# Performance work log

Hardware: AMD Instinct MI355X
Metric: run time of the kernel (lower is better)

Reference implementation:

```python
import jax, jax.numpy as jnp
import numpy as np

B, N, H, D, F = 32, 128, 256, 256, 512   # batch, nodes, gru hidden, latent dim, mlp hidden
SUP = 0.5                                 # ancestor_suppression_strength
EPS = 1e-6


def _gru(x, h, Wx, Wh, bx, bh):
    """torch.nn.GRUCell math; x,h: [..., H]."""
    gx = x @ Wx + bx
    gh = h @ Wh + bh
    rx, ux, nx = jnp.split(gx, 3, axis=-1)
    rh, uh, nh = jnp.split(gh, 3, axis=-1)
    r = jax.nn.sigmoid(rx + rh)
    u = jax.nn.sigmoid(ux + uh)
    n = jnp.tanh(nx + r * nh)
    return (1.0 - u) * n + u * h


def setup_inputs() -> dict:
    key = jax.random.key(0)
    ks = jax.random.split(key, 12)
    rn = lambda k, shape, fan: jax.random.normal(k, shape, jnp.float32) * (fan ** -0.5)
    return {
        "z": jax.random.normal(ks[0], (B, D), jnp.float32),
        "targets": jax.random.randint(ks[1], (B, N, N), 0, 2, jnp.int32),
        "W_init": rn(ks[2], (D, H), D),
        "b_init": jnp.zeros((H,), jnp.float32),
        "Wx": rn(ks[3], (H, 3 * H), H),
        "Wh": rn(ks[4], (H, 3 * H), H),
        "bx": jnp.zeros((3 * H,), jnp.float32),
        "bh": jnp.zeros((3 * H,), jnp.float32),
        "W1": rn(ks[5], (2 * H + D, F), 2 * H + D),
        "b1": jnp.zeros((F,), jnp.float32),
        "W2": rn(ks[6], (F, 1), F),
        "b2": jnp.zeros((1,), jnp.float32),
    }


def reference(z, targets, W_init, b_init, Wx, Wh, bx, bh, W1, b1, W2, b2):
    # teacher-forcing link targets: strictly lower-triangular (parents have smaller index)
    tgt = jnp.tril(targets.astype(jnp.float32), k=-1)  # [B,N,N]
    idx = jnp.arange(N)

    def decode_one(z1, t1):  # z1:[D], t1:[N,N]
        h0 = jnp.tanh(z1 @ W_init + b_init)                      # decoder_init: z -> node-0 state
        states0 = jnp.zeros((N, H), jnp.float32).at[0].set(h0)
        A0 = jnp.zeros((N, N), jnp.float32)                      # ancestor bitset: A[i,j]=1 iff j ancestor of i

        def step(carry, t):
            states, A, ll = carry
            m = (idx < t).astype(jnp.float32)                    # existing-node mask
            pooled = (states * m[:, None]).sum(0) / m.sum()      # mean aggregation
            h_prov = _gru(pooled, h0, Wx, Wh, bx, bh)            # provisional new-node state
            # parent logits: MLP([h_new, h_j, z]) for every existing node j
            feat = jnp.concatenate([jnp.broadcast_to(h_prov, (N, H)), states,
                                    jnp.broadcast_to(z1, (N, D))], axis=-1)   # [N, 2H+D]
            logits = (jax.nn.relu(feat @ W1 + b1) @ W2 + b2)[:, 0]            # [N]
            row = t1[t]                                          # teacher-forced parents of node t
            anc = jnp.minimum(row @ A, 1.0)                      # j already ancestor of a chosen parent
            q = jnp.clip(jax.nn.sigmoid(logits) * (1.0 - SUP * anc), EPS, 1.0 - EPS)
            ll = ll + (m * (row * jnp.log(q) + (1.0 - row) * jnp.log1p(-q))).sum()
            A = A.at[t].set(jnp.minimum(row + row @ A, 1.0))     # ancestors(t) = parents U their ancestors
            states = states.at[t].set(h_prov)
            m2 = (idx <= t).astype(jnp.float32)[:, None]
            pooled2 = (states * m2).sum(0) / m2.sum()
            upd = _gru(jnp.broadcast_to(pooled2, (N, H)), states, Wx, Wh, bx, bh)
            states = m2 * upd + (1.0 - m2) * states              # propagate info among generated nodes
            return (states, A, ll), None

        (states, A, ll), _ = jax.lax.scan(step, (states0, A0, jnp.zeros((), jnp.float32)),
                                          jnp.arange(1, N))
        return t1, ll                                            # link matrix (teacher forced), log-likelihood

    L, ll = jax.vmap(decode_one)(z, tgt)
    return L, ll
```

## Files before the change

kernel.cpp:

```cpp
#include <hip/hip_runtime.h>
#include <hip/hip_bf16.h>
#include <math.h>

#define Bz 32
#define Nn 128
#define Hh 256
#define Dd 256
#define Ff 512
#define Gg 768
#define NT 512

typedef short v8s __attribute__((ext_vector_type(8)));
typedef float f4  __attribute__((ext_vector_type(4)));
#define MFMA(a,b,c) __builtin_amdgcn_mfma_f32_16x16x32_bf16(a,b,c,0,0,0)

#define WS_H0    0
#define WS_GH0   (WS_H0 + Bz*Hh)
#define WS_ZW1   (WS_GH0 + Bz*Gg)
#define WS_GXP   (WS_ZW1 + Bz*Ff)
#define WS_LOGP  (WS_GXP + Bz*2*8*Gg)
#define WS_BAR   (WS_LOGP + Bz*2*8*Nn)
#define WS_XS    (WS_BAR + Bz*32)
#define WS_WB    (WS_XS + Bz*16384)

#define SM_SW    0
#define SM_SST   81920
#define SM_NLDS  147456
#define SM_GXF   155648
#define SM_HPF   158720
#define SM_GX2   159232
#define SM_GHT   159616
#define SM_BASE  160000
#define SM_BHS   160256
#define SM_PSN   160640
#define SM_LOGI  160768
#define SM_RBIT  161280
#define SM_ANCW  161312
#define SM_AMASK 161376
#define SMEM_SZ  163424

__device__ __forceinline__ unsigned short f2bf(float x) {
  unsigned u = __float_as_uint(x);
  u = u + 0x7fffu + ((u >> 16) & 1u);
  return (unsigned short)(u >> 16);
}
__device__ __forceinline__ unsigned pack2(float e, float o) {
  return (unsigned)f2bf(e) | ((unsigned)f2bf(o) << 16);
}
__device__ __forceinline__ unsigned pkbf(float x, float y) {
  __hip_bfloat162 h = __float22bfloat162_rn(make_float2(x, y));
  union { __hip_bfloat162 h; unsigned u; } c; c.h = h; return c.u;
}
__device__ __forceinline__ float bf2f(unsigned short s) {
  return __uint_as_float(((unsigned)s) << 16);
}
__device__ __forceinline__ float sigm(float x) { return 1.0f / (1.0f + __expf(-x)); }
__device__ __forceinline__ float tanh_fast(float x) { return 2.0f / (1.0f + __expf(-2.0f*x)) - 1.0f; }
__device__ __forceinline__ v8s u4v(uint4 q) { union { uint4 q; v8s v; } c; c.q = q; return c.v; }

__device__ __forceinline__ void ast32(unsigned* p, unsigned v) {
  __hip_atomic_store(p, v, __ATOMIC_RELAXED, __HIP_MEMORY_SCOPE_AGENT);
}
__device__ __forceinline__ unsigned ald32(const unsigned* p) {
  return __hip_atomic_load(p, __ATOMIC_RELAXED, __HIP_MEMORY_SCOPE_AGENT);
}
__device__ __forceinline__ void ast64(unsigned long long* p, unsigned long long v) {
  __hip_atomic_store(p, v, __ATOMIC_RELAXED, __HIP_MEMORY_SCOPE_AGENT);
}
__device__ __forceinline__ unsigned long long ald64(const unsigned long long* p) {
  return __hip_atomic_load(p, __ATOMIC_RELAXED, __HIP_MEMORY_SCOPE_AGENT);
}

__device__ __forceinline__ void bbar(unsigned* cnt, unsigned& seq)
{
  __builtin_amdgcn_s_waitcnt(0x0F70);
  __syncthreads();
  seq += 8;
  if (threadIdx.x == 0) {
    __hip_atomic_fetch_add(cnt, 1u, __ATOMIC_RELAXED, __HIP_MEMORY_SCOPE_AGENT);
    while (__hip_atomic_load(cnt, __ATOMIC_RELAXED, __HIP_MEMORY_SCOPE_AGENT) < seq)
      __builtin_amdgcn_s_sleep(1);
  }
  __syncthreads();
}

__global__ void __launch_bounds__(256) prep_init(
    const int* __restrict__ tg, const float* __restrict__ Wx,
    const float* __restrict__ Wh, const float* __restrict__ W1,
    float* __restrict__ ws, float* __restrict__ out)
{
  const int stride = gridDim.x * blockDim.x;
  const int t0 = blockIdx.x * blockDim.x + threadIdx.x;

  for (int i = t0; i < Bz*Nn*Nn; i += stride) {
    int col = i & (Nn-1), row = (i >> 7) & (Nn-1);
    out[i] = (col < row) ? (float)tg[i] : 0.0f;
  }
  for (int i = t0; i < Bz; i += stride) out[Bz*Nn*Nn + i] = 0.0f;

  unsigned* BARu = (unsigned*)(ws + WS_BAR);
  for (int i = t0; i < Bz*32; i += stride) BARu[i] = 0u;

  unsigned* Wb = (unsigned*)(ws + WS_WB);
  for (int i = t0; i < 160*2048; i += stride) {
    int jw = i & 3, l = (i >> 2) & 63, ks = (i >> 8) & 7, nt = i >> 11;
    int k = ks*32 + (l >> 4)*8 + 2*jw;
    int n16 = l & 15;
    float lo, hi;
    if (nt < 48)       { int c = nt*16 + n16;        lo = Wh[k*Gg + c];      hi = Wh[(k+1)*Gg + c]; }
    else if (nt < 80)  { int f = (nt-48)*16 + n16;   lo = W1[(Hh+k)*Ff + f]; hi = W1[(Hh+k+1)*Ff + f]; }
    else if (nt < 128) { int c = (nt-80)*16 + n16;   lo = Wx[k*Gg + c];      hi = Wx[(k+1)*Gg + c]; }
    else               { int f = (nt-128)*16 + n16;  lo = W1[k*Ff + f];      hi = W1[(k+1)*Ff + f]; }
    Wb[i] = pack2(lo, hi);
  }
}

__global__ void __launch_bounds__(256) prep_batch(
    const float* __restrict__ z, const float* __restrict__ Wi,
    const float* __restrict__ bi, const float* __restrict__ Wh,
    const float* __restrict__ bh, const float* __restrict__ W1,
    float* __restrict__ ws)
{
  const int b = blockIdx.x, tid = threadIdx.x;
  __shared__ float zs[Dd], h0s[Hh];
  zs[tid] = z[b*Dd + tid];
  __syncthreads();
  float acc = bi[tid];
  for (int d = 0; d < Dd; ++d) acc = fmaf(zs[d], Wi[d*Hh + tid], acc);
  const float h0 = tanhf(acc);
  h0s[tid] = h0;
  ws[WS_H0 + b*Hh + tid] = h0;
  __syncthreads();
  for (int g = tid; g < Gg; g += 256) {
    float a = bh[g];
    for (int h = 0; h < Hh; ++h) a = fmaf(h0s[h], Wh[h*Gg + g], a);
    ws[WS_GH0 + b*Gg + g] = a;
  }
  for (int f = tid; f < Ff; f += 256) {
    float a = 0.0f;
    for (int d = 0; d < Dd; ++d) a = fmaf(zs[d], W1[(2*Hh + d)*Ff + f], a);
    ws[WS_ZW1 + b*Ff + f] = a;
  }
}

__device__ __forceinline__ void G_mfma(const unsigned short* SST, const uint4* SW4,
    int mt0, bool do1, int lane, f4* acc)
{
  #pragma unroll
  for (int ks = 0; ks < 8; ++ks) {
    const v8s a0 = *(const v8s*)(SST + (mt0*8 + ks)*512 + lane*8);
    const v8s w0 = u4v(SW4[(0*8 + ks)*64 + lane]);
    const v8s w1 = u4v(SW4[(1*8 + ks)*64 + lane]);
    const v8s w2 = u4v(SW4[(2*8 + ks)*64 + lane]);
    const v8s w3 = u4v(SW4[(3*8 + ks)*64 + lane]);
    const v8s w4 = u4v(SW4[(4*8 + ks)*64 + lane]);
    const v8s w5 = u4v(SW4[(5*8 + ks)*64 + lane]);
    acc[0] = MFMA(a0,w0,acc[0]); acc[1] = MFMA(a0,w1,acc[1]);
    acc[2] = MFMA(a0,w2,acc[2]); acc[3] = MFMA(a0,w3,acc[3]);
    acc[4] = MFMA(a0,w4,acc[4]); acc[5] = MFMA(a0,w5,acc[5]);
    if (do1) {
      const v8s a1 = *(const v8s*)(SST + ((mt0+1)*8 + ks)*512 + lane*8);
      acc[6]  = MFMA(a1,w0,acc[6]);  acc[7]  = MFMA(a1,w1,acc[7]);
      acc[8]  = MFMA(a1,w2,acc[8]);  acc[9]  = MFMA(a1,w3,acc[9]);
      acc[10] = MFMA(a1,w4,acc[10]); acc[11] = MFMA(a1,w5,acc[11]);
    }
  }
}

__device__ __forceinline__ void G_epi(const f4* ac, int mt, int t, int r,
    int quad, int c16, int lane, const float* GX2, const float* BHS,
    const unsigned short* SST, unsigned short* NLDS, float* PSN)
{
  #pragma unroll
  for (int ct = 0; ct < 2; ++ct) {
    const int hcl = ct*16 + c16;
    const f4 cr = ac[0 + ct], cu = ac[2 + ct], cn = ac[4 + ct];
    const float gxr = GX2[hcl], gxu = GX2[32+hcl], gxn = GX2[64+hcl];
    const float bhr = BHS[hcl], bhu = BHS[32+hcl], bhn = BHS[64+hcl];
    float colsum = 0.0f;
    #pragma unroll
    for (int rg = 0; rg < 4; ++rg) {
      const int row = mt*16 + quad*4 + rg;
      if (row < t) {
        const int spi = ((hcl>>3)*16 + quad*4 + rg)*8 + (hcl & 7);
        const float old = bf2f(SST[(mt*8 + r)*512 + spi]);
        const float rv = sigm(gxr + cr[rg] + bhr);
        const float uv = sigm(gxu + cu[rg] + bhu);
        const float nv = tanh_fast(gxn + rv*(cn[rg] + bhn));
        const float ns = (1.0f-uv)*nv + uv*old;
        NLDS[mt*512 + spi] = f2bf(ns);
        colsum += ns;
      }
    }
    colsum += __shfl_down(colsum, 16);
    colsum += __shfl_down(colsum, 32);
    if (lane < 16) atomicAdd(&PSN[ct*16 + lane], colsum);
  }
}

__device__ __forceinline__ void L_mfma(const unsigned short* SST, const uint4* SW4,
    int mt0, bool do1, int lane, f4* acc)
{
  #pragma unroll
  for (int ks = 0; ks < 8; ++ks) {
    const v8s a0 = *(const v8s*)(SST + (mt0*8 + ks)*512 + lane*8);
    const v8s c0 = u4v(SW4[(6*8 + ks)*64 + lane]);
    const v8s c1 = u4v(SW4[(7*8 + ks)*64 + lane]);
    const v8s c2 = u4v(SW4[(8*8 + ks)*64 + lane]);
    const v8s c3 = u4v(SW4[(9*8 + ks)*64 + lane]);
    acc[0] = MFMA(a0,c0,acc[0]); acc[1] = MFMA(a0,c1,acc[1]);
    acc[2] = MFMA(a0,c2,acc[2]); acc[3] = MFMA(a0,c3,acc[3]);
    if (do1) {
      const v8s a1 = *(const v8s*)(SST + ((mt0+1)*8 + ks)*512 + lane*8);
      acc[4] = MFMA(a1,c0,acc[4]); acc[5] = MFMA(a1,c1,acc[5]);
      acc[6] = MFMA(a1,c2,acc[6]); acc[7] = MFMA(a1,c3,acc[7]);
    }
  }
}

__device__ __forceinline__ void L_epi(const f4* ac, int mt, int t,
    int quad, int c16, const float* BASE, const float* w2r, float* LOGI)
{
  #pragma unroll
  for (int rg = 0; rg < 4; ++rg) {
    float v = fmaxf(ac[0][rg] + BASE[c16],    0.0f)*w2r[0]
            + fmaxf(ac[1][rg] + BASE[16+c16], 0.0f)*w2r[1]
            + fmaxf(ac[2][rg] + BASE[32+c16], 0.0f)*w2r[2]
            + fmaxf(ac[3][rg] + BASE[48+c16], 0.0f)*w2r[3];
    v += __shfl_xor(v, 1); v += __shfl_xor(v, 2);
    v += __shfl_xor(v, 4); v += __shfl_xor(v, 8);
    const int row = mt*16 + quad*4 + rg;
    if (c16 == 0 && row < t) atomicAdd(&LOGI[row], v);
  }
}

__global__ void __launch_bounds__(NT) decoder_main(
    const int* __restrict__ tg,
    const float* __restrict__ bx, const float* __restrict__ bh,
    const float* __restrict__ b1, const float* __restrict__ W2,
    const float* __restrict__ b2,
    float* __restrict__ ws, float* __restrict__ out)
{
  const int blk = blockIdx.x;
  const int b = blk & 31, r = blk >> 5;
  const int tid = threadIdx.x;
  const int lane = tid & 63, wv = tid >> 6;
  const int c16 = lane & 15, quad = lane >> 4;

  extern __shared__ char smem[];
  uint4* SW4 = (uint4*)(smem + SM_SW);
  unsigned short* SST = (unsigned short*)(smem + SM_SST);
  unsigned long long* SST64 = (unsigned long long*)(smem + SM_SST);
  unsigned short* NLDS = (unsigned short*)(smem + SM_NLDS);
  unsigned* NLDSu = (unsigned*)(smem + SM_NLDS);
  unsigned long long* NLDS64 = (unsigned long long*)(smem + SM_NLDS);
  float* GXF  = (float*)(smem + SM_GXF);
  unsigned short* HPF = (unsigned short*)(smem + SM_HPF);
  float* GX2  = (float*)(smem + SM_GX2);
  float* GHT  = (float*)(smem + SM_GHT);
  float* BASE = (float*)(smem + SM_BASE);
  float* BHS  = (float*)(smem + SM_BHS);
  float* PSN  = (float*)(smem + SM_PSN);
  float* LOGI = (float*)(smem + SM_LOGI);
  unsigned* RBIT  = (unsigned*)(smem + SM_RBIT);
  unsigned* ANCW  = (unsigned*)(smem + SM_ANCW);
  unsigned* AMASK = (unsigned*)(smem + SM_AMASK);

  const float* __restrict__ h0g  = ws + WS_H0  + b*Hh;
  const float* __restrict__ gh0g = ws + WS_GH0 + b*Gg;
  const float* __restrict__ zW1g = ws + WS_ZW1 + b*Ff;
  unsigned* GXPb = (unsigned*)(ws + WS_GXP) + b*2*8*Gg;
  unsigned* LOGPb = (unsigned*)(ws + WS_LOGP) + b*2*8*Nn;
  unsigned* bar = (unsigned*)(ws + WS_BAR) + b*32;
  unsigned long long* XS64 = (unsigned long long*)(ws + WS_XS) + b*8192;
  const uint4* WB4 = (const uint4*)(ws + WS_WB);

  for (int i = tid; i < 16384; i += NT) ((unsigned*)SST)[i] = 0u;
  for (int i = tid; i < 4096; i += NT) NLDSu[i] = 0u;
  for (int i = tid; i < 5120; i += NT) {
    const int lt = i >> 9, q = i & 511;
    int gt;
    if (lt < 6) { const int gate = lt >> 1, tt = lt & 1; gt = gate*16 + 2*r + tt; }
    else        { gt = 48 + 4*r + (lt - 6); }
    SW4[lt*512 + q] = WB4[gt*512 + q];
  }
  for (int i = tid; i < Nn*4; i += NT) AMASK[i] = 0u;
  if (tid < 96) BHS[tid] = bh[(tid >> 5)*256 + 32*r + (tid & 31)];
  float w2r[4];
  #pragma unroll
  for (int ft = 0; ft < 4; ++ft) w2r[ft] = W2[64*r + ft*16 + c16];
  const float b2v = b2[0];
  float p_bx[3][4], p_gh[3][4], p_h0[4];
  if (wv >= 6) {
    #pragma unroll
    for (int k = 0; k < 4; ++k) {
      const int c = 4*lane + k;
      p_h0[k] = h0g[c];
      #pragma unroll
      for (int g3 = 0; g3 < 3; ++g3) {
        p_bx[g3][k] = bx[g3*256 + c];
        p_gh[g3][k] = gh0g[g3*256 + c];
      }
    }
  }
  unsigned bseq = 0;
  __syncthreads();
  if (tid < Hh) {
    const int c = tid;
    SST[(c>>5)*512 + ((c>>3)&3)*128 + (c&7)] = f2bf(h0g[c]);
  }
  if (tid < 32) PSN[tid] = h0g[32*r + tid];
  __syncthreads();
  {
    union { unsigned u[4]; v8s v; } cv;
    const float4 a0 = *(const float4*)(PSN + quad*8);
    const float4 a1 = *(const float4*)(PSN + quad*8 + 4);
    cv.u[0] = pkbf(a0.x, a0.y); cv.u[1] = pkbf(a0.z, a0.w);
    cv.u[2] = pkbf(a1.x, a1.y); cv.u[3] = pkbf(a1.z, a1.w);
    const v8s avp = cv.v;
    unsigned* GXPw = GXPb + 1*8*Gg + r*Gg;
    #pragma unroll
    for (int k2 = 0; k2 < 6; ++k2) {
      const int nt = wv*6 + k2;
      f4 c = {0.0f,0.0f,0.0f,0.0f};
      c = MFMA(avp, u4v(WB4[(80 + nt)*512 + r*64 + lane]), c);
      if (quad == 0) ast32(GXPw + nt*16 + c16, __float_as_uint(c[0]));
    }
  }
  if (tid < 128) ast64(XS64 + r*128 + tid, SST64[r*128 + tid]);
  bbar(bar, bseq);

  for (int t = 1; t < Nn; ++t) {
    const int tpar = t & 1;
    const float invt  = 1.0f / (float)t;
    const float invt1 = 1.0f / (float)(t + 1);
    const int Mr   = (t + 15) >> 4;
    const int Mtot = (t + 16) >> 4;
    const int mtc  = t >> 4;
    const int nG = (Mr + 1) >> 1, nL = (Mr + 1) >> 1;
    const int njobs = nG + nL;

    for (int i = tid; i < Mr*1024; i += NT) {
      if (((i >> 7) & 7) != r) SST64[i] = ald64(XS64 + i);
    }
    if (tid < 384) {
      const unsigned long long* GXPr =
          (const unsigned long long*)(GXPb + tpar*8*Gg);
      float s0 = 0.0f, s1 = 0.0f;
      #pragma unroll
      for (int rr = 0; rr < 8; ++rr) {
        const unsigned long long v = ald64(GXPr + rr*384 + tid);
        s0 += __uint_as_float((unsigned)v);
        s1 += __uint_as_float((unsigned)(v >> 32));
      }
      GXF[2*tid]   = s0;
      GXF[2*tid+1] = s1;
    } else {
      const int j = tid - 384;
      const int val = (j < t) ? tg[b*Nn*Nn + t*Nn + j] : 0;
      const unsigned long long bal = __ballot(val != 0);
      if (lane == 0) {
        RBIT[tpar*4 + (wv-6)*2]     = (unsigned)bal;
        RBIT[tpar*4 + (wv-6)*2 + 1] = (unsigned)(bal >> 32);
      }
      LOGI[j] = 0.0f;
      if (j < 32) PSN[j] = 0.0f;
      unsigned m0=0,m1=0,m2=0,m3=0;
      if (j < t && val != 0) {
        m0 = AMASK[j*4+0]; m1 = AMASK[j*4+1];
        m2 = AMASK[j*4+2]; m3 = AMASK[j*4+3];
      }
      #pragma unroll
      for (int off = 1; off < 64; off <<= 1) {
        m0 |= __shfl_xor(m0, off); m1 |= __shfl_xor(m1, off);
        m2 |= __shfl_xor(m2, off); m3 |= __shfl_xor(m3, off);
      }
      if (lane == 0) {
        unsigned* aw = ANCW + tpar*8 + (wv-6)*4;
        aw[0] = m0; aw[1] = m1; aw[2] = m2; aw[3] = m3;
      }
    }
    __syncthreads();

    f4 acc[12];
    #pragma unroll
    for (int i = 0; i < 12; ++i) acc[i] = (f4){0.0f,0.0f,0.0f,0.0f};
    bool haveA = false, d1A = false; int kindA = 0, mtA = 0;
    if (wv < 6) {
      if (wv < njobs && wv < 6) {
        haveA = true;
        if (wv < nG) { kindA = 0; mtA = 2*wv;       d1A = (mtA + 1 < Mr); }
        else         { kindA = 1; mtA = 2*(wv-nG);  d1A = (mtA + 1 < Mr); }
        if (kindA == 0) G_mfma(SST, SW4, mtA, d1A, lane, acc);
        else            L_mfma(SST, SW4, mtA, d1A, lane, acc);
      }
    } else {
      if (wv == 6 && lane < 4)
        AMASK[t*4 + lane] = RBIT[tpar*4 + lane] | ANCW[tpar*8 + lane] | ANCW[tpar*8 + 4 + lane];
      if ((t & 15) == 0) {
        for (int q = tid - 384; q < 256; q += 128) NLDSu[mtc*256 + q] = 0u;
      }
      float hp[4];
      #pragma unroll
      for (int k = 0; k < 4; ++k) {
        const int c = 4*lane + k;
        const float rv = sigm(GXF[c]*invt       + p_bx[0][k] + p_gh[0][k]);
        const float uv = sigm(GXF[256+c]*invt   + p_bx[1][k] + p_gh[1][k]);
        const float nv = tanh_fast(GXF[512+c]*invt + p_bx[2][k] + rv*p_gh[2][k]);
        hp[k] = (1.0f - uv)*nv + uv*p_h0[k];
      }
      uint2 pk;
      pk.x = pack2(hp[0], hp[1]); pk.y = pack2(hp[2], hp[3]);
      *(uint2*)((unsigned short*)HPF + 4*lane) = pk;
      v8s av[8];
      #pragma unroll
      for (int ks = 0; ks < 8; ++ks) av[ks] = *(const v8s*)(HPF + ks*32 + quad*8);
      for (int j = wv - 6; j < 16; j += 2) {
        f4 c = {0.0f,0.0f,0.0f,0.0f};
        if (j < 6) {
          #pragma unroll
          for (int ks = 0; ks < 8; ++ks) c = MFMA(av[ks], u4v(SW4[(j*8 + ks)*64 + lane]), c);
          if (quad == 0) GHT[(j>>1)*32 + (j&1)*16 + c16] = c[0];
        } else if (j < 12) {
          const int jx = j - 6, g = jx >> 1, tt = jx & 1;
          const uint4* Bp = WB4 + (80 + g*16 + 2*r + tt)*512 + lane;
          #pragma unroll
          for (int ks = 0; ks < 8; ++ks) c = MFMA(av[ks], u4v(Bp[ks*64]), c);
          if (quad == 0) {
            const int col = g*256 + 32*r + tt*16 + c16;
            GX2[g*32 + tt*16 + c16] = (c[0] + GXF[col])*invt1 + bx[col];
          }
        } else {
          const int ft = j - 12;
          const uint4* Bp = WB4 + (128 + 4*r + ft)*512 + lane;
          #pragma unroll
          for (int ks = 0; ks < 8; ++ks) c = MFMA(av[ks], u4v(Bp[ks*64]), c);
          if (quad == 0) {
            const int f = 64*r + ft*16 + c16;
            BASE[ft*16 + c16] = c[0] + zW1g[f] + b1[f];
          }
        }
      }
    }
    __syncthreads();

    if (wv < 6) {
      if (haveA) {
        if (kindA == 0) {
          G_epi(acc,     mtA,   t, r, quad, c16, lane, GX2, BHS, SST, NLDS, PSN);
          if (d1A) G_epi(acc+6, mtA+1, t, r, quad, c16, lane, GX2, BHS, SST, NLDS, PSN);
        } else {
          L_epi(acc,     mtA,   t, quad, c16, BASE, w2r, LOGI);
          if (d1A) L_epi(acc+4, mtA+1, t, quad, c16, BASE, w2r, LOGI);
        }
      }
      if (wv < 2) {
        const int jB = 6 + wv;
        if (jB < njobs) {
          const int mtB = 2*(jB - nG);
          const bool d1B = (mtB + 1 < Mr);
          f4 acc2[8];
          #pragma unroll
          for (int i = 0; i < 8; ++i) acc2[i] = (f4){0.0f,0.0f,0.0f,0.0f};
          L_mfma(SST, SW4, mtB, d1B, lane, acc2);
          L_epi(acc2,     mtB,   t, quad, c16, BASE, w2r, LOGI);
          if (d1B) L_epi(acc2+4, mtB+1, t, quad, c16, BASE, w2r, LOGI);
        }
      }
    } else if (wv == 6 && lane < 32) {
      const int hcl = lane;
      const float rv = sigm(GX2[hcl]    + GHT[hcl]    + BHS[hcl]);
      const float uv = sigm(GX2[32+hcl] + GHT[32+hcl] + BHS[32+hcl]);
      const float nv = tanh_fast(GX2[64+hcl] + rv*(GHT[64+hcl] + BHS[64+hcl]));
      const float old = bf2f(HPF[32*r + hcl]);
      const float ns = (1.0f - uv)*nv + uv*old;
      const int spi = ((hcl>>3)*16 + (t & 15))*8 + (hcl & 7);
      NLDS[mtc*512 + spi] = f2bf(ns);
      atomicAdd(&PSN[hcl], ns);
    }
    __syncthreads();

    {
      union { unsigned u[4]; v8s v; } cv;
      const float4 a0 = *(const float4*)(PSN + quad*8);
      const float4 a1 = *(const float4*)(PSN + quad*8 + 4);
      cv.u[0] = pkbf(a0.x, a0.y); cv.u[1] = pkbf(a0.z, a0.w);
      cv.u[2] = pkbf(a1.x, a1.y); cv.u[3] = pkbf(a1.z, a1.w);
      const v8s avp = cv.v;
      unsigned* GXPw = GXPb + ((t+1)&1)*8*Gg + r*Gg;
      #pragma unroll
      for (int k2 = 0; k2 < 6; ++k2) {
        const int nt = wv*6 + k2;
        f4 c = {0.0f,0.0f,0.0f,0.0f};
        c = MFMA(avp, u4v(WB4[(80 + nt)*512 + r*64 + lane]), c);
        if (quad == 0) ast32(GXPw + nt*16 + c16, __float_as_uint(c[0]));
      }
    }
    for (int i = tid; i < Mtot*128; i += NT) {
      const int mt = i >> 7, q = i & 127;
      const unsigned long long v = NLDS64[i];
      ast64(XS64 + (mt*8 + r)*128 + q, v);
      SST64[(mt*8 + r)*128 + q] = v;
    }
    if (tid < 64)
      ast64((unsigned long long*)LOGPb + tpar*512 + r*64 + tid,
            ((const unsigned long long*)LOGI)[tid]);
    if (t > 1 && r == ((t - 1) & 7)) {
      const int pp = (t - 1) & 1;
      float term = 0.0f;
      if (tid < (t - 1)) {
        float lsum = b2v;
        const unsigned* Lp = LOGPb + pp*1024;
        #pragma unroll
        for (int rr = 0; rr < 8; ++rr)
          lsum += __uint_as_float(ald32(Lp + rr*Nn + tid));
        const int w = tid >> 5;
        const unsigned av_ = ANCW[pp*8 + w] | ANCW[pp*8 + 4 + w];
        const float anc = (float)((av_ >> (tid & 31)) & 1u);
        float q = sigm(lsum) * (1.0f - 0.5f*anc);
        q = fminf(fmaxf(q, 1e-6f), 1.0f - 1e-6f);
        const unsigned rb = (RBIT[pp*4 + w] >> (tid & 31)) & 1u;
        term = rb ? logf(q) : log1pf(-q);
      }
      if (wv < 2) {
        #pragma unroll
        for (int off = 32; off; off >>= 1) term += __shfl_down(term, off);
        if (lane == 0) atomicAdd(&out[Bz*Nn*Nn + b], term);
      }
    }
    bbar(bar, bseq);
  }

  if (r == 7) {
    const int tl = Nn - 1;
    const int pp = tl & 1;
    float term = 0.0f;
    if (tid < tl) {
      float lsum = b2v;
      const unsigned* Lp = LOGPb + pp*1024;
      #pragma unroll
      for (int rr = 0; rr < 8; ++rr)
        lsum += __uint_as_float(ald32(Lp + rr*Nn + tid));
      const int w = tid >> 5;
      const unsigned av_ = ANCW[pp*8 + w] | ANCW[pp*8 + 4 + w];
      const float anc = (float)((av_ >> (tid & 31)) & 1u);
      float q = sigm(lsum) * (1.0f - 0.5f*anc);
      q = fminf(fmaxf(q, 1e-6f), 1.0f - 1e-6f);
      const unsigned rb = (RBIT[pp*4 + w] >> (tid & 31)) & 1u;
      term = rb ? logf(q) : log1pf(-q);
    }
    if (wv < 2) {
      #pragma unroll
      for (int off = 32; off; off >>= 1) term += __shfl_down(term, off);
      if (lane == 0) atomicAdd(&out[Bz*Nn*Nn + b], term);
    }
  }
}

extern "C" void kernel_launch(void* const* d_in, const int* in_sizes, int n_in,
                              void* d_out, int out_size, void* d_ws, size_t ws_size,
                              hipStream_t stream)
{
  const float* z  = (const float*)d_in[0];
  const int*   tg = (const int*)  d_in[1];
  const float* Wi = (const float*)d_in[2];
  const float* bi = (const float*)d_in[3];
  const float* Wx = (const float*)d_in[4];
  const float* Wh = (const float*)d_in[5];
  const float* bx = (const float*)d_in[6];
  const float* bh = (const float*)d_in[7];
  const float* W1 = (const float*)d_in[8];
  const float* b1 = (const float*)d_in[9];
  const float* W2 = (const float*)d_in[10];
  const float* b2 = (const float*)d_in[11];
  float* out = (float*)d_out;
  float* ws  = (float*)d_ws;

  hipFuncSetAttribute((const void*)decoder_main,
                      hipFuncAttributeMaxDynamicSharedMemorySize, SMEM_SZ);

  hipLaunchKernelGGL(prep_init, dim3(512), dim3(256), 0, stream, tg, Wx, Wh, W1, ws, out);
  hipLaunchKernelGGL(prep_batch, dim3(Bz), dim3(256), 0, stream, z, Wi, bi, Wh, bh, W1, ws);

  void* args[] = { (void*)&tg, (void*)&bx, (void*)&bh, (void*)&b1,
                   (void*)&W2, (void*)&b2, (void*)&ws, (void*)&out };
  hipLaunchCooperativeKernel((void*)decoder_main, dim3(256), dim3(NT),
                             args, SMEM_SZ, stream);
}
```

Measured before the change: 1.968 ms.

## Replace atomic group barrier with per-block flags and double-buffered state exchange

Replaces the counter-based inter-block barrier with per-block step flags polled by one wave, and double-buffers the cross-block state exchange buffer so blocks can proceed without a full rendezvous. It also prefetches teacher-forcing rows into shared memory one step ahead, spreads the log-likelihood computation across all blocks, and rebalances MFMA work across waves. The aim is to cut per-step synchronisation latency across the 128 sequential steps, at the cost of extra workspace and more delicate memory-ordering reasoning with relaxed atomics.

```diff
diff --git a/kernel.cpp b/kernel.cpp
--- a/kernel.cpp
+++ b/kernel.cpp
@@ -21,7 +21,7 @@
 #define WS_LOGP  (WS_GXP + Bz*2*8*Gg)
 #define WS_BAR   (WS_LOGP + Bz*2*8*Nn)
 #define WS_XS    (WS_BAR + Bz*32)
-#define WS_WB    (WS_XS + Bz*16384)
+#define WS_WB    (WS_XS + Bz*32768)
 
 #define SM_SW    0
 #define SM_SST   81920
@@ -34,10 +34,11 @@
 #define SM_BHS   160256
 #define SM_PSN   160640
 #define SM_LOGI  160768
-#define SM_RBIT  161280
-#define SM_ANCW  161312
-#define SM_AMASK 161376
-#define SMEM_SZ  163424
+#define SM_TGR   161280
+#define SM_RBIT  161536
+#define SM_ANCW  161568
+#define SM_AMASK 161600
+#define SMEM_SZ  163648
 
 __device__ __forceinline__ unsigned short f2bf(float x) {
   unsigned u = __float_as_uint(x);
@@ -71,17 +72,14 @@
   return __hip_atomic_load(p, __ATOMIC_RELAXED, __HIP_MEMORY_SCOPE_AGENT);
 }
 
-__device__ __forceinline__ void bbar(unsigned* cnt, unsigned& seq)
-{
-  __builtin_amdgcn_s_waitcnt(0x0F70);
-  __syncthreads();
-  seq += 8;
-  if (threadIdx.x == 0) {
-    __hip_atomic_fetch_add(cnt, 1u, __ATOMIC_RELAXED, __HIP_MEMORY_SCOPE_AGENT);
-    while (__hip_atomic_load(cnt, __ATOMIC_RELAXED, __HIP_MEMORY_SCOPE_AGENT) < seq)
-      __builtin_amdgcn_s_sleep(1);
-  }
-  __syncthreads();
+__device__ __forceinline__ void waitflags(const unsigned* FLG, int lane, int r, unsigned tgt)
+{
+  const bool watch = (lane < 8) && (lane != r);
+  for (;;) {
+    const unsigned f = watch ? ald32(FLG + lane) : 0xFFFFFFFFu;
+    if (__ballot(f >= tgt) == 0xFFFFFFFFFFFFFFFFull) break;
+  }
+  __atomic_signal_fence(__ATOMIC_ACQUIRE);
 }
 
 __global__ void __launch_bounds__(256) prep_init(
@@ -234,6 +232,33 @@
   }
 }
 
+__device__ __forceinline__ void ll_gen(int tg_, int r, int lane, float b2v,
+    const unsigned* LOGPb, const unsigned* RBIT, const unsigned* ANCW,
+    float* out_ll)
+{
+  const int pp = tg_ & 1;
+  const int row = 16*r + (lane >> 2);
+  float term = 0.0f;
+  if (row < tg_) {
+    const unsigned* Lp = LOGPb + pp*1024;
+    const int rr = (lane & 3)*2;
+    float s = __uint_as_float(ald32(Lp + rr*128 + row))
+            + __uint_as_float(ald32(Lp + (rr+1)*128 + row));
+    s += __shfl_xor(s, 1); s += __shfl_xor(s, 2);
+    if ((lane & 3) == 0) {
+      const int w = row >> 5;
+      const float anc = (float)((ANCW[pp*4 + w] >> (row & 31)) & 1u);
+      float q = sigm(b2v + s) * (1.0f - 0.5f*anc);
+      q = fminf(fmaxf(q, 1e-6f), 1.0f - 1e-6f);
+      const unsigned rb = (RBIT[pp*4 + w] >> (row & 31)) & 1u;
+      term = rb ? logf(q) : log1pf(-q);
+    }
+  }
+  #pragma unroll
+  for (int off = 1; off < 64; off <<= 1) term += __shfl_xor(term, off);
+  if (lane == 0) atomicAdd(out_ll, term);
+}
+
 __global__ void __launch_bounds__(NT) decoder_main(
     const int* __restrict__ tg,
     const float* __restrict__ bx, const float* __restrict__ bh,
@@ -262,6 +287,7 @@
   float* BHS  = (float*)(smem + SM_BHS);
   float* PSN  = (float*)(smem + SM_PSN);
   float* LOGI = (float*)(smem + SM_LOGI);
+  unsigned char* TGRu = (unsigned char*)(smem + SM_TGR);
   unsigned* RBIT  = (unsigned*)(smem + SM_RBIT);
   unsigned* ANCW  = (unsigned*)(smem + SM_ANCW);
   unsigned* AMASK = (unsigned*)(smem + SM_AMASK);
@@ -271,9 +297,10 @@
   const float* __restrict__ zW1g = ws + WS_ZW1 + b*Ff;
   unsigned* GXPb = (unsigned*)(ws + WS_GXP) + b*2*8*Gg;
   unsigned* LOGPb = (unsigned*)(ws + WS_LOGP) + b*2*8*Nn;
-  unsigned* bar = (unsigned*)(ws + WS_BAR) + b*32;
-  unsigned long long* XS64 = (unsigned long long*)(ws + WS_XS) + b*8192;
+  unsigned* FLG = (unsigned*)(ws + WS_BAR) + b*32;
+  unsigned long long* XS64b = (unsigned long long*)(ws + WS_XS) + b*16384;
   const uint4* WB4 = (const uint4*)(ws + WS_WB);
+  float* out_ll = out + Bz*Nn*Nn + b;
 
   for (int i = tid; i < 16384; i += NT) ((unsigned*)SST)[i] = 0u;
   for (int i = tid; i < 4096; i += NT) NLDSu[i] = 0u;
@@ -286,24 +313,36 @@
   }
   for (int i = tid; i < Nn*4; i += NT) AMASK[i] = 0u;
   if (tid < 96) BHS[tid] = bh[(tid >> 5)*256 + 32*r + (tid & 31)];
+  if (tid < 128) TGRu[128 + tid] = (unsigned char)tg[b*Nn*Nn + 1*Nn + tid];
   float w2r[4];
   #pragma unroll
   for (int ft = 0; ft < 4; ++ft) w2r[ft] = W2[64*r + ft*16 + c16];
   const float b2v = b2[0];
   float p_bx[3][4], p_gh[3][4], p_h0[4];
-  if (wv >= 6) {
+  #pragma unroll
+  for (int k = 0; k < 4; ++k) {
+    const int c = 4*lane + k;
+    p_h0[k] = h0g[c];
     #pragma unroll
-    for (int k = 0; k < 4; ++k) {
-      const int c = 4*lane + k;
-      p_h0[k] = h0g[c];
-      #pragma unroll
-      for (int g3 = 0; g3 < 3; ++g3) {
-        p_bx[g3][k] = bx[g3*256 + c];
-        p_gh[g3][k] = gh0g[g3*256 + c];
-      }
-    }
-  }
-  unsigned bseq = 0;
+    for (int g3 = 0; g3 < 3; ++g3) {
+      p_bx[g3][k] = bx[g3*256 + c];
+      p_gh[g3][k] = gh0g[g3*256 + c];
+    }
+  }
+  int colj[2]; float auxj[2];
+  #pragma unroll
+  for (int jj = 0; jj < 2; ++jj) {
+    const int j = 2*wv + jj;
+    colj[jj] = 0; auxj[jj] = 0.0f;
+    if (j >= 6 && j < 12) {
+      const int jx = j - 6, g = jx >> 1, tt = jx & 1;
+      const int col = g*256 + 32*r + tt*16 + c16;
+      colj[jj] = col; auxj[jj] = bx[col];
+    } else if (j >= 12) {
+      const int ft = j - 12, f = 64*r + ft*16 + c16;
+      auxj[jj] = zW1g[f] + b1[f];
+    }
+  }
   __syncthreads();
   if (tid < Hh) {
     const int c = tid;
@@ -327,11 +366,13 @@
       if (quad == 0) ast32(GXPw + nt*16 + c16, __float_as_uint(c[0]));
     }
   }
-  if (tid < 128) ast64(XS64 + r*128 + tid, SST64[r*128 + tid]);
-  bbar(bar, bseq);
+  if (tid < 128) ast64(XS64b + r*128 + tid, SST64[r*128 + tid]);
+  __builtin_amdgcn_s_waitcnt(0x0F70);
+  __syncthreads();
+  if (tid == 0) { __atomic_signal_fence(__ATOMIC_RELEASE); ast32(FLG + r, 1u); }
 
   for (int t = 1; t < Nn; ++t) {
-    const int tpar = t & 1;
+    const int tp = t & 1;
     const float invt  = 1.0f / (float)t;
     const float invt1 = 1.0f / (float)(t + 1);
     const int Mr   = (t + 15) >> 4;
@@ -340,35 +381,47 @@
     const int nG = (Mr + 1) >> 1, nL = (Mr + 1) >> 1;
     const int njobs = nG + nL;
 
-    for (int i = tid; i < Mr*1024; i += NT) {
-      if (((i >> 7) & 7) != r) SST64[i] = ald64(XS64 + i);
-    }
+    waitflags(FLG, lane, r, (unsigned)t);
+
     if (tid < 384) {
-      const unsigned long long* GXPr =
-          (const unsigned long long*)(GXPb + tpar*8*Gg);
+      const unsigned long long* GXPr = (const unsigned long long*)(GXPb + tp*8*Gg);
+      unsigned long long g[8];
+      #pragma unroll
+      for (int rr = 0; rr < 8; ++rr) g[rr] = ald64(GXPr + rr*384 + tid);
       float s0 = 0.0f, s1 = 0.0f;
       #pragma unroll
       for (int rr = 0; rr < 8; ++rr) {
-        const unsigned long long v = ald64(GXPr + rr*384 + tid);
-        s0 += __uint_as_float((unsigned)v);
-        s1 += __uint_as_float((unsigned)(v >> 32));
+        s0 += __uint_as_float((unsigned)g[rr]);
+        s1 += __uint_as_float((unsigned)(g[rr] >> 32));
       }
       GXF[2*tid]   = s0;
       GXF[2*tid+1] = s1;
-    } else {
-      const int j = tid - 384;
-      const int val = (j < t) ? tg[b*Nn*Nn + t*Nn + j] : 0;
-      const unsigned long long bal = __ballot(val != 0);
+    }
+    if (tid < 448) {
+      const unsigned long long* XSr = XS64b + ((t-1)&1)*8192;
+      for (int i = tid; i < Mr*1024; i += 448) {
+        if (((i >> 7) & 7) != r) SST64[i] = ald64(XSr + i);
+      }
+    }
+    if (wv == 6) {
+      const int v0 = TGRu[tp*128 + lane];
+      const int v1 = TGRu[tp*128 + lane + 64];
+      const unsigned long long bal0 = __ballot(lane < t && v0);
+      const unsigned long long bal1 = __ballot((lane + 64) < t && v1);
       if (lane == 0) {
-        RBIT[tpar*4 + (wv-6)*2]     = (unsigned)bal;
-        RBIT[tpar*4 + (wv-6)*2 + 1] = (unsigned)(bal >> 32);
-      }
-      LOGI[j] = 0.0f;
-      if (j < 32) PSN[j] = 0.0f;
+        RBIT[tp*4+0] = (unsigned)bal0; RBIT[tp*4+1] = (unsigned)(bal0 >> 32);
+        RBIT[tp*4+2] = (unsigned)bal1; RBIT[tp*4+3] = (unsigned)(bal1 >> 32);
+      }
+      LOGI[lane] = 0.0f; LOGI[lane+64] = 0.0f;
+      if (lane < 32) PSN[lane] = 0.0f;
       unsigned m0=0,m1=0,m2=0,m3=0;
-      if (j < t && val != 0) {
-        m0 = AMASK[j*4+0]; m1 = AMASK[j*4+1];
-        m2 = AMASK[j*4+2]; m3 = AMASK[j*4+3];
+      if (lane < t && v0) {
+        m0 = AMASK[lane*4+0]; m1 = AMASK[lane*4+1];
+        m2 = AMASK[lane*4+2]; m3 = AMASK[lane*4+3];
+      }
+      if (lane + 64 < t && v1) {
+        m0 |= AMASK[(lane+64)*4+0]; m1 |= AMASK[(lane+64)*4+1];
+        m2 |= AMASK[(lane+64)*4+2]; m3 |= AMASK[(lane+64)*4+3];
       }
       #pragma unroll
       for (int off = 1; off < 64; off <<= 1) {
@@ -376,46 +429,37 @@
         m2 |= __shfl_xor(m2, off); m3 |= __shfl_xor(m3, off);
       }
       if (lane == 0) {
-        unsigned* aw = ANCW + tpar*8 + (wv-6)*4;
-        aw[0] = m0; aw[1] = m1; aw[2] = m2; aw[3] = m3;
-      }
-    }
+        ANCW[tp*4+0] = m0; ANCW[tp*4+1] = m1;
+        ANCW[tp*4+2] = m2; ANCW[tp*4+3] = m3;
+      }
+    }
+    if (wv == 7 && t > 1) ll_gen(t-1, r, lane, b2v, LOGPb, RBIT, ANCW, out_ll);
     __syncthreads();
 
-    f4 acc[12];
-    #pragma unroll
-    for (int i = 0; i < 12; ++i) acc[i] = (f4){0.0f,0.0f,0.0f,0.0f};
-    bool haveA = false, d1A = false; int kindA = 0, mtA = 0;
-    if (wv < 6) {
-      if (wv < njobs && wv < 6) {
-        haveA = true;
-        if (wv < nG) { kindA = 0; mtA = 2*wv;       d1A = (mtA + 1 < Mr); }
-        else         { kindA = 1; mtA = 2*(wv-nG);  d1A = (mtA + 1 < Mr); }
-        if (kindA == 0) G_mfma(SST, SW4, mtA, d1A, lane, acc);
-        else            L_mfma(SST, SW4, mtA, d1A, lane, acc);
-      }
-    } else {
-      if (wv == 6 && lane < 4)
-        AMASK[t*4 + lane] = RBIT[tpar*4 + lane] | ANCW[tpar*8 + lane] | ANCW[tpar*8 + 4 + lane];
-      if ((t & 15) == 0) {
-        for (int q = tid - 384; q < 256; q += 128) NLDSu[mtc*256 + q] = 0u;
-      }
+    {
       float hp[4];
+      const float* gr = GXF + 4*lane;
       #pragma unroll
       for (int k = 0; k < 4; ++k) {
-        const int c = 4*lane + k;
-        const float rv = sigm(GXF[c]*invt       + p_bx[0][k] + p_gh[0][k]);
-        const float uv = sigm(GXF[256+c]*invt   + p_bx[1][k] + p_gh[1][k]);
-        const float nv = tanh_fast(GXF[512+c]*invt + p_bx[2][k] + rv*p_gh[2][k]);
+        const float rv = sigm(gr[k]*invt       + p_bx[0][k] + p_gh[0][k]);
+        const float uv = sigm(gr[256+k]*invt   + p_bx[1][k] + p_gh[1][k]);
+        const float nv = tanh_fast(gr[512+k]*invt + p_bx[2][k] + rv*p_gh[2][k]);
         hp[k] = (1.0f - uv)*nv + uv*p_h0[k];
       }
       uint2 pk;
       pk.x = pack2(hp[0], hp[1]); pk.y = pack2(hp[2], hp[3]);
-      *(uint2*)((unsigned short*)HPF + 4*lane) = pk;
+      *(uint2*)(HPF + 4*lane) = pk;
+      if (wv == 0 && lane < 4)
+        AMASK[t*4 + lane] = RBIT[tp*4 + lane] | ANCW[tp*4 + lane];
+      if (wv == 1 && (t & 15) == 0) {
+        for (int q = lane; q < 256; q += 64) NLDSu[mtc*256 + q] = 0u;
+      }
       v8s av[8];
       #pragma unroll
       for (int ks = 0; ks < 8; ++ks) av[ks] = *(const v8s*)(HPF + ks*32 + quad*8);
-      for (int j = wv - 6; j < 16; j += 2) {
+      #pragma unroll
+      for (int jj = 0; jj < 2; ++jj) {
+        const int j = 2*wv + jj;
         f4 c = {0.0f,0.0f,0.0f,0.0f};
         if (j < 6) {
           #pragma unroll
@@ -426,48 +470,40 @@
           const uint4* Bp = WB4 + (80 + g*16 + 2*r + tt)*512 + lane;
           #pragma unroll
           for (int ks = 0; ks < 8; ++ks) c = MFMA(av[ks], u4v(Bp[ks*64]), c);
-          if (quad == 0) {
-            const int col = g*256 + 32*r + tt*16 + c16;
-            GX2[g*32 + tt*16 + c16] = (c[0] + GXF[col])*invt1 + bx[col];
-          }
+          if (quad == 0) GX2[g*32 + tt*16 + c16] = (c[0] + GXF[colj[jj]])*invt1 + auxj[jj];
         } else {
           const int ft = j - 12;
           const uint4* Bp = WB4 + (128 + 4*r + ft)*512 + lane;
           #pragma unroll
           for (int ks = 0; ks < 8; ++ks) c = MFMA(av[ks], u4v(Bp[ks*64]), c);
-          if (quad == 0) {
-            const int f = 64*r + ft*16 + c16;
-            BASE[ft*16 + c16] = c[0] + zW1g[f] + b1[f];
-          }
+          if (quad == 0) BASE[ft*16 + c16] = c[0] + auxj[jj];
         }
       }
     }
     __syncthreads();
 
-    if (wv < 6) {
-      if (haveA) {
-        if (kindA == 0) {
-          G_epi(acc,     mtA,   t, r, quad, c16, lane, GX2, BHS, SST, NLDS, PSN);
-          if (d1A) G_epi(acc+6, mtA+1, t, r, quad, c16, lane, GX2, BHS, SST, NLDS, PSN);
-        } else {
-          L_epi(acc,     mtA,   t, quad, c16, BASE, w2r, LOGI);
-          if (d1A) L_epi(acc+4, mtA+1, t, quad, c16, BASE, w2r, LOGI);
-        }
-      }
-      if (wv < 2) {
-        const int jB = 6 + wv;
-        if (jB < njobs) {
-          const int mtB = 2*(jB - nG);
-          const bool d1B = (mtB + 1 < Mr);
-          f4 acc2[8];
-          #pragma unroll
-          for (int i = 0; i < 8; ++i) acc2[i] = (f4){0.0f,0.0f,0.0f,0.0f};
-          L_mfma(SST, SW4, mtB, d1B, lane, acc2);
-          L_epi(acc2,     mtB,   t, quad, c16, BASE, w2r, LOGI);
-          if (d1B) L_epi(acc2+4, mtB+1, t, quad, c16, BASE, w2r, LOGI);
-        }
-      }
-    } else if (wv == 6 && lane < 32) {
+    if (wv < njobs) {
+      if (wv < nG) {
+        const int mt0 = 2*wv;
+        const bool do1 = (mt0 + 1 < Mr);
+        f4 acc[12];
+        #pragma unroll
+        for (int i = 0; i < 12; ++i) acc[i] = (f4){0.0f,0.0f,0.0f,0.0f};
+        G_mfma(SST, SW4, mt0, do1, lane, acc);
+        G_epi(acc, mt0, t, r, quad, c16, lane, GX2, BHS, SST, NLDS, PSN);
+        if (do1) G_epi(acc+6, mt0+1, t, r, quad, c16, lane, GX2, BHS, SST, NLDS, PSN);
+      } else {
+        const int mt0 = 2*(wv - nG);
+        const bool do1 = (mt0 + 1 < Mr);
+        f4 acc[8];
+        #pragma unroll
+        for (int i = 0; i < 8; ++i) acc[i] = (f4){0.0f,0.0f,0.0f,0.0f};
+        L_mfma(SST, SW4, mt0, do1, lane, acc);
+        L_epi(acc, mt0, t, quad, c16, BASE, w2r, LOGI);
+        if (do1) L_epi(acc+4, mt0+1, t, quad, c16, BASE, w2r, LOGI);
+      }
+    }
+    if (wv == 7 && lane < 32) {
       const int hcl = lane;
       const float rv = sigm(GX2[hcl]    + GHT[hcl]    + BHS[hcl]);
       const float uv = sigm(GX2[32+hcl] + GHT[32+hcl] + BHS[32+hcl]);
@@ -496,64 +532,31 @@
         if (quad == 0) ast32(GXPw + nt*16 + c16, __float_as_uint(c[0]));
       }
     }
-    for (int i = tid; i < Mtot*128; i += NT) {
-      const int mt = i >> 7, q = i & 127;
-      const unsigned long long v = NLDS64[i];
-      ast64(XS64 + (mt*8 + r)*128 + q, v);
-      SST64[(mt*8 + r)*128 + q] = v;
+    {
+      unsigned long long* XSw = XS64b + tp*8192;
+      for (int i = tid; i < Mtot*128; i += NT) {
+        const int mt = i >> 7, q = i & 127;
+        const unsigned long long v = NLDS64[i];
+        ast64(XSw + (mt*8 + r)*128 + q, v);
+        SST64[(mt*8 + r)*128 + q] = v;
+      }
     }
     if (tid < 64)
-      ast64((unsigned long long*)LOGPb + tpar*512 + r*64 + tid,
+      ast64((unsigned long long*)LOGPb + tp*512 + r*64 + tid,
             ((const unsigned long long*)LOGI)[tid]);
-    if (t > 1 && r == ((t - 1) & 7)) {
-      const int pp = (t - 1) & 1;
-      float term = 0.0f;
-      if (tid < (t - 1)) {
-        float lsum = b2v;
-        const unsigned* Lp = LOGPb + pp*1024;
-        #pragma unroll
-        for (int rr = 0; rr < 8; ++rr)
-          lsum += __uint_as_float(ald32(Lp + rr*Nn + tid));
-        const int w = tid >> 5;
-        const unsigned av_ = ANCW[pp*8 + w] | ANCW[pp*8 + 4 + w];
-        const float anc = (float)((av_ >> (tid & 31)) & 1u);
-        float q = sigm(lsum) * (1.0f - 0.5f*anc);
-        q = fminf(fmaxf(q, 1e-6f), 1.0f - 1e-6f);
-        const unsigned rb = (RBIT[pp*4 + w] >> (tid & 31)) & 1u;
-        term = rb ? logf(q) : log1pf(-q);
-      }
-      if (wv < 2) {
-        #pragma unroll
-        for (int off = 32; off; off >>= 1) term += __shfl_down(term, off);
-        if (lane == 0) atomicAdd(&out[Bz*Nn*Nn + b], term);
-      }
-    }
-    bbar(bar, bseq);
-  }
-
-  if (r == 7) {
-    const int tl = Nn - 1;
-    const int pp = tl & 1;
-    float term = 0.0f;
-    if (tid < tl) {
-      float lsum = b2v;
-      const unsigned* Lp = LOGPb + pp*1024;
-      #pragma unroll
-      for (int rr = 0; rr < 8; ++rr)
-        lsum += __uint_as_float(ald32(Lp + rr*Nn + tid));
-      const int w = tid >> 5;
-      const unsigned av_ = ANCW[pp*8 + w] | ANCW[pp*8 + 4 + w];
-      const float anc = (float)((av_ >> (tid & 31)) & 1u);
-      float q = sigm(lsum) * (1.0f - 0.5f*anc);
-      q = fminf(fmaxf(q, 1e-6f), 1.0f - 1e-6f);
-      const unsigned rb = (RBIT[pp*4 + w] >> (tid & 31)) & 1u;
-      term = rb ? logf(q) : log1pf(-q);
-    }
-    if (wv < 2) {
-      #pragma unroll
-      for (int off = 32; off; off >>= 1) term += __shfl_down(term, off);
-      if (lane == 0) atomicAdd(&out[Bz*Nn*Nn + b], term);
-    }
+    if (wv == 7 && t + 1 < Nn) {
+      const int base = b*Nn*Nn + (t+1)*Nn;
+      TGRu[((t+1)&1)*128 + lane]      = (unsigned char)tg[base + lane];
+      TGRu[((t+1)&1)*128 + lane + 64] = (unsigned char)tg[base + lane + 64];
+    }
+    __builtin_amdgcn_s_waitcnt(0x0F70);
+    __syncthreads();
+    if (tid == 0) { __atomic_signal_fence(__ATOMIC_RELEASE); ast32(FLG + r, (unsigned)(t + 1)); }
+  }
+
+  if (wv == 7) {
+    waitflags(FLG, lane, r, (unsigned)Nn);
+    ll_gen(Nn - 1, r, lane, b2v, LOGPb, RBIT, ANCW, out_ll);
   }
 }
 
```

Result: slower. 2.341 ms (+18.9%).
